# Optimization experiments

Measured on AMD Instinct MI355X. Metric: run time of the kernel, lower is better.

Reference implementation:

```python
import jax, jax.numpy as jnp
import numpy as np

B, K, G, C = 64, 4000, 200, 91
LAMBDA_BOX, LAMBDA_CLS, LAMBDA_OBJ = 5.0, 1.0, 1.0
EPS = 1e-9


def _make_boxes(key, lead_shape):
    k1, k2 = jax.random.split(key)
    tl = jax.random.uniform(k1, lead_shape + (2,)) * 0.7
    wh = jax.random.uniform(k2, lead_shape + (2,)) * 0.29 + 0.01
    return jnp.concatenate([tl, tl + wh], axis=-1)


def setup_inputs() -> dict:
    key = jax.random.key(0)
    ks = jax.random.split(key, 6)
    pred_boxes = _make_boxes(ks[0], (B, K))
    pred_obj_logits = jax.random.normal(ks[1], (B, K), dtype=jnp.float32)
    pred_cls_logits = jax.random.normal(ks[2], (B, K, C), dtype=jnp.float32)
    gt_boxes = _make_boxes(ks[3], (B, G))
    gt_labels = jax.random.randint(ks[4], (B, G), 0, C)
    n_gt = jax.random.randint(ks[5], (B,), 1, G + 1)
    gt_mask = jnp.arange(G)[None, :] < n_gt[:, None]
    return dict(pred_boxes=pred_boxes, pred_obj_logits=pred_obj_logits,
                pred_cls_logits=pred_cls_logits, gt_boxes=gt_boxes,
                gt_labels=gt_labels, gt_mask=gt_mask)


def _area(x):
    return jnp.clip(x[..., 2] - x[..., 0], 0.0) * jnp.clip(x[..., 3] - x[..., 1], 0.0)


def _pairwise_iou(a, b):
    # a: (K,4), b: (G,4) -> (K,G)
    tl = jnp.maximum(a[:, None, :2], b[None, :, :2])
    br = jnp.minimum(a[:, None, 2:], b[None, :, 2:])
    wh = jnp.clip(br - tl, 0.0)
    inter = wh[..., 0] * wh[..., 1]
    union = jnp.clip(_area(a)[:, None] + _area(b)[None, :] - inter, EPS)
    return inter / union


def _ciou_loss(pb, gb):
    # pb, gb: (M,4) matched pairs; elementwise CIoU loss = 1 - CIoU
    tl = jnp.maximum(pb[:, :2], gb[:, :2])
    br = jnp.minimum(pb[:, 2:], gb[:, 2:])
    wh = jnp.clip(br - tl, 0.0)
    inter = wh[:, 0] * wh[:, 1]
    iou = inter / jnp.clip(_area(pb) + _area(gb) - inter, EPS)
    px = (pb[:, 0] + pb[:, 2]) * 0.5
    py = (pb[:, 1] + pb[:, 3]) * 0.5
    tx = (gb[:, 0] + gb[:, 2]) * 0.5
    ty = (gb[:, 1] + gb[:, 3]) * 0.5
    rho2 = (px - tx) ** 2 + (py - ty) ** 2
    etl = jnp.minimum(pb[:, :2], gb[:, :2])
    ebr = jnp.maximum(pb[:, 2:], gb[:, 2:])
    c2 = jnp.clip((ebr[:, 0] - etl[:, 0]) ** 2 + (ebr[:, 1] - etl[:, 1]) ** 2, EPS)
    pw = jnp.clip(pb[:, 2] - pb[:, 0], EPS)
    ph = jnp.clip(pb[:, 3] - pb[:, 1], EPS)
    tw = jnp.clip(gb[:, 2] - gb[:, 0], EPS)
    th = jnp.clip(gb[:, 3] - gb[:, 1], EPS)
    v = (4.0 / jnp.pi ** 2) * (jnp.arctan(tw / th) - jnp.arctan(pw / ph)) ** 2
    alpha = jax.lax.stop_gradient(v / (1.0 - iou + v + EPS))  # torch.no_grad
    return 1.0 - (iou - rho2 / c2 - alpha * v)


def _greedy_match(iou0):
    # iou0: (K,G), invalid gt columns pre-masked to -1. Fixed min(K,G)-step
    # argmax-and-mask scan reproducing the torch greedy loop (break -> valid=False).
    Gd = iou0.shape[1]
    steps = min(iou0.shape[0], Gd)

    def step(m, _):
        flat = jnp.argmax(m)
        p = flat // Gd
        g = flat % Gd
        valid = m.reshape(-1)[flat] >= 0.0
        m2 = m.at[p, :].set(-1.0).at[:, g].set(-1.0)
        return jnp.where(valid, m2, m), (p, g, valid)

    _, (ps, gs, vs) = jax.lax.scan(step, iou0, None, length=steps)
    return ps, gs, vs


def _per_batch(pred_b, cls_b, gt_b, labels_b, mask_b):
    iou = jax.lax.stop_gradient(_pairwise_iou(pred_b, gt_b))  # matching is non-diff (.item() in torch)
    iou = jnp.where(mask_b[None, :], iou, -1.0)
    ps, gs, vs = _greedy_match(iou)
    vf = vs.astype(pred_b.dtype)
    n = jnp.sum(vf)
    denom = jnp.maximum(n, 1.0)
    pb = pred_b[ps]
    gb = gt_b[gs]
    lbox = jnp.sum(_ciou_loss(pb, gb) * vf) / denom
    logp = jax.nn.log_softmax(cls_b[ps], axis=-1)
    lce = -jnp.take_along_axis(logp, labels_b[gs][:, None], axis=1)[:, 0]
    lcls = jnp.sum(lce * vf) / denom
    obj_tgt = jnp.zeros((pred_b.shape[0],), pred_b.dtype).at[
        jnp.where(vs, ps, pred_b.shape[0])].set(1.0, mode='drop')
    return lbox, lcls, obj_tgt, n > 0.0


def reference(pred_boxes, pred_obj_logits, pred_cls_logits, gt_boxes, gt_labels, gt_mask):
    lbox_b, lcls_b, obj_tgt, has = jax.vmap(_per_batch)(
        pred_boxes, pred_cls_logits, gt_boxes, gt_labels, gt_mask)
    hf = has.astype(pred_boxes.dtype)
    nb = jnp.maximum(jnp.sum(hf), 1.0)
    loss_box = jnp.sum(lbox_b * hf) / nb
    loss_cls = jnp.sum(lcls_b * hf) / nb
    # BCEWithLogits(mean): softplus(x) - t*x
    loss_obj = jnp.mean(jax.nn.softplus(pred_obj_logits) - obj_tgt * pred_obj_logits)
    total = LAMBDA_BOX * loss_box + LAMBDA_CLS * loss_cls + LAMBDA_OBJ * loss_obj
    return total, loss_box, loss_cls, loss_obj
```

## Files before the change

kernel.cpp:

```cpp
#include <hip/hip_runtime.h>
#include <math.h>

#define B_ 64
#define K_ 4000
#define G_ 200
#define C_ 91
#define EPS_ 1e-9f
#define NW_ 16
#define DEPTH_ 32
typedef unsigned long long ull;

#define WS_FLAG 0
#define WS_PART 256
#define WS_TOP 65536

__device__ __forceinline__ float box_area(float4 a) {
#pragma clang fp contract(off)
  return fmaxf(a.z - a.x, 0.f) * fmaxf(a.w - a.y, 0.f);
}

__device__ __forceinline__ float iou_ab(float4 a, float aA, float4 b, float aB) {
#pragma clang fp contract(off)
  float tlx = fmaxf(a.x, b.x), tly = fmaxf(a.y, b.y);
  float brx = fminf(a.z, b.z), bry = fminf(a.w, b.w);
  float w = fmaxf(brx - tlx, 0.f), h = fmaxf(bry - tly, 0.f);
  float inter = w * h;
  float uni = fmaxf(aA + aB - inter, EPS_);
  return inter / uni;
}

__device__ __forceinline__ float ciou_loss(float4 p, float4 g) {
  float tlx = fmaxf(p.x, g.x), tly = fmaxf(p.y, g.y);
  float brx = fminf(p.z, g.z), bry = fminf(p.w, g.w);
  float w = fmaxf(brx - tlx, 0.f), h = fmaxf(bry - tly, 0.f);
  float inter = w * h;
  float areaP = fmaxf(p.z - p.x, 0.f) * fmaxf(p.w - p.y, 0.f);
  float areaG = fmaxf(g.z - g.x, 0.f) * fmaxf(g.w - g.y, 0.f);
  float iou = inter / fmaxf(areaP + areaG - inter, EPS_);
  float px = (p.x + p.z) * 0.5f, py = (p.y + p.w) * 0.5f;
  float tx = (g.x + g.z) * 0.5f, ty = (g.y + g.w) * 0.5f;
  float rho2 = (px - tx) * (px - tx) + (py - ty) * (py - ty);
  float ex = fmaxf(p.z, g.z) - fminf(p.x, g.x);
  float ey = fmaxf(p.w, g.w) - fminf(p.y, g.y);
  float c2 = fmaxf(ex * ex + ey * ey, EPS_);
  float pw = fmaxf(p.z - p.x, EPS_), ph = fmaxf(p.w - p.y, EPS_);
  float tw = fmaxf(g.z - g.x, EPS_), th = fmaxf(g.w - g.y, EPS_);
  float dat = atanf(tw / th) - atanf(pw / ph);
  float v = (4.0f / (float)(M_PI * M_PI)) * dat * dat;
  float alpha = v / ((1.f - iou) + v + EPS_);
  return 1.f - (iou - rho2 / c2 - alpha * v);
}

__global__ void kdetect(const unsigned char* m8, int* flag) {
  int b = threadIdx.x;
  int ok = 1;
  const unsigned char* r = m8 + b * G_;
  if (r[0] != 1) ok = 0;
  int seen0 = 0;
  for (int g = 0; g < G_; ++g) {
    unsigned char c = r[g];
    if (c > 1) { ok = 0; break; }
    if (c == 0) seen0 = 1;
    else if (seen0) { ok = 0; break; }
  }
  int all = __all(ok);
  if (b == 0) *flag = all ? 1 : 0;
}

__device__ __forceinline__ float block_sum(float v, float* s_red) {
  for (int off = 32; off > 0; off >>= 1) v += __shfl_xor(v, off);
  int lane = threadIdx.x & 63, wid = threadIdx.x >> 6;
  if (lane == 0) s_red[wid] = v;
  __syncthreads();
  float r = 0.f;
  if (wid == 0) {
    float t = (lane < NW_) ? s_red[lane] : 0.f;
    for (int off = 32; off > 0; off >>= 1) t += __shfl_xor(t, off);
    r = t;
  }
  __syncthreads();
  return r;
}

__device__ __forceinline__ void merge4_stage(ull& v0, ull& v1, ull& v2, ull& v3,
                                             int off) {
  ull w0 = __shfl_xor(v0, off), w1 = __shfl_xor(v1, off);
  ull w2 = __shfl_xor(v2, off), w3 = __shfl_xor(v3, off);
  ull t0 = v0 > w3 ? v0 : w3;
  ull t1 = v1 > w2 ? v1 : w2;
  ull t2 = v2 > w1 ? v2 : w1;
  ull t3 = v3 > w0 ? v3 : w0;
  ull x;
  if (t2 > t0) { x = t0; t0 = t2; t2 = x; }
  if (t3 > t1) { x = t1; t1 = t3; t3 = x; }
  if (t1 > t0) { x = t0; t0 = t1; t1 = x; }
  if (t3 > t2) { x = t2; t2 = t3; t3 = x; }
  v0 = t0; v1 = t1; v2 = t2; v3 = t3;
}

#define TOP4_INS(key, t0, t1, t2, t3)                   \
  if ((key) > t3) {                                     \
    t3 = (key);                                         \
    ull tmp_;                                           \
    if (t3 > t2) { tmp_ = t2; t2 = t3; t3 = tmp_; }     \
    if (t2 > t1) { tmp_ = t1; t1 = t2; t2 = tmp_; }     \
    if (t1 > t0) { tmp_ = t0; t0 = t1; t1 = tmp_; }     \
  }

__device__ __forceinline__ void rank_extract(ull t0, ull t1, ull t2, ull t3,
                                             ull* dst, int lane) {
  int r0 = 0, r1 = 0, r2 = 0, r3 = 0;
  for (int i = 0; i < 64; ++i) {
    ull o0 = __shfl(t0, i), o1 = __shfl(t1, i);
    ull o2 = __shfl(t2, i), o3 = __shfl(t3, i);
    r0 += (o0 > t0) + (o1 > t0) + (o2 > t0) + (o3 > t0);
    r1 += (o0 > t1) + (o1 > t1) + (o2 > t1) + (o3 > t1);
    r2 += (o0 > t2) + (o1 > t2) + (o2 > t2) + (o3 > t2);
    r3 += (o0 > t3) + (o1 > t3) + (o2 > t3) + (o3 > t3);
  }
  int cut = (t3 != 0ull) ? (r3 + 1) : 0x7FFFFFFF;
  int nc = (t0 != 0ull) + (t1 != 0ull) + (t2 != 0ull) + (t3 != 0ull);
  for (int off = 32; off > 0; off >>= 1) {
    int oc = __shfl_xor(cut, off);
    cut = (oc < cut) ? oc : cut;
    nc += __shfl_xor(nc, off);
  }
  const int Lf = (cut < DEPTH_) ? cut : DEPTH_;
  const int zstart = (Lf < nc) ? Lf : nc;
  if (t0 != 0ull && r0 < Lf) dst[r0] = t0;
  if (t1 != 0ull && r1 < Lf) dst[r1] = t1;
  if (t2 != 0ull && r2 < Lf) dst[r2] = t2;
  if (t3 != 0ull && r3 < Lf) dst[r3] = t3;
  for (int o = lane; o < DEPTH_; o += 64)
    if (o >= zstart) dst[o] = 0ull;
}

__global__ __launch_bounds__(1024) void kinit(const float* __restrict__ pred_boxes,
                                              const float* __restrict__ gt_boxes,
                                              const void* __restrict__ gt_mask,
                                              char* __restrict__ ws) {
  const int wv = blockIdx.x * 16 + (threadIdx.x >> 6);
  const int lane = threadIdx.x & 63;
  const int b = wv / 100, j = wv - 100 * b;
  const int c0 = 2 * j, c1 = 2 * j + 1;
  const int msk8 = *(const int*)(ws + WS_FLAG);
  const float4* p4 = (const float4*)pred_boxes + (size_t)b * K_;
  const float4* g4 = (const float4*)gt_boxes + (size_t)b * G_;

  int vA, vB;
  if (msk8) {
    vA = ((const unsigned char*)gt_mask)[(size_t)b * G_ + c0] != 0;
    vB = ((const unsigned char*)gt_mask)[(size_t)b * G_ + c1] != 0;
  } else {
    vA = ((const int*)gt_mask)[(size_t)b * G_ + c0] != 0;
    vB = ((const int*)gt_mask)[(size_t)b * G_ + c1] != 0;
  }
  if (!(vA | vB)) return;

  float4 gbA, gbB;
  float gAA = 0.f, gAB = 0.f;
  if (vA) { gbA = g4[c0]; gAA = box_area(gbA); }
  if (vB) { gbB = g4[c1]; gAB = box_area(gbB); }

  ull a0 = 0, a1 = 0, a2 = 0, a3 = 0;
  ull b0 = 0, b1 = 0, b2 = 0, b3 = 0;
#pragma unroll 4
  for (int k = lane; k < K_; k += 64) {
    float4 pb = p4[k];
    float ar = box_area(pb);
    if (vA) {
      float iou = iou_ab(pb, ar, gbA, gAA);
      ull e = ((ull)__float_as_uint(iou) << 12) | (ull)(4095 - k);
      TOP4_INS(e, a0, a1, a2, a3);
    }
    if (vB) {
      float iou = iou_ab(pb, ar, gbB, gAB);
      ull e = ((ull)__float_as_uint(iou) << 12) | (ull)(4095 - k);
      TOP4_INS(e, b0, b1, b2, b3);
    }
  }
  ull* wtop = (ull*)(ws + WS_TOP);
  if (vA) rank_extract(a0, a1, a2, a3, wtop + ((size_t)b * G_ + c0) * DEPTH_, lane);
  if (vB) rank_extract(b0, b1, b2, b3, wtop + ((size_t)b * G_ + c1) * DEPTH_, lane);
}

__global__ __launch_bounds__(1024) void kmerged(
    const float* __restrict__ pred_boxes, const float* __restrict__ obj_logits,
    const float* __restrict__ cls_logits, const float* __restrict__ gt_boxes,
    const int* __restrict__ gt_labels, const void* __restrict__ gt_mask,
    char* __restrict__ ws) {
  __shared__ float s_gx[G_], s_gy[G_], s_gz[G_], s_gw[G_], s_garea[G_];
  __shared__ unsigned char s_valid[G_];
  __shared__ unsigned char s_rowused[4096];
  __shared__ ull s_tlkey[G_][DEPTH_ + 1];
  __shared__ unsigned short s_tlrow[G_][DEPTH_ + 1];
  __shared__ int s_mp[G_];
  __shared__ unsigned short s_mg[G_];
  __shared__ int s_cnt;
  __shared__ float s_red[NW_];
  const int b = blockIdx.x;
  const int tid = threadIdx.x, lane = tid & 63, wid = tid >> 6;
  const int msk8 = *(const int*)(ws + WS_FLAG);
  const float4* p4 = (const float4*)pred_boxes + (size_t)b * K_;
  const float4* g4 = (const float4*)gt_boxes + (size_t)b * G_;
  const ull* wtop = (const ull*)(ws + WS_TOP);

  for (int g = tid; g < G_; g += 1024) {
    float4 gb = g4[g];
    s_gx[g] = gb.x; s_gy[g] = gb.y; s_gz[g] = gb.z; s_gw[g] = gb.w;
    s_garea[g] = box_area(gb);
    int v;
    if (msk8) v = ((const unsigned char*)gt_mask)[(size_t)b * G_ + g] != 0;
    else      v = ((const int*)gt_mask)[(size_t)b * G_ + g] != 0;
    s_valid[g] = (unsigned char)v;
  }
  for (int k = tid; k < 4096; k += 1024) s_rowused[k] = 0;
  __syncthreads();
  for (int i = tid; i < G_ * DEPTH_; i += 1024) {
    int col = i >> 5, o = i & 31;
    ull v = s_valid[col] ? wtop[(size_t)b * G_ * DEPTH_ + i] : 0ull;
    s_tlkey[col][o] = v;
    s_tlrow[col][o] = v ? (unsigned short)(4095 - (int)((v >> 12) & 0xFFF))
                        : (unsigned short)0xFFFF;
  }
  __syncthreads();

  if (wid == 0) {
    ull key0 = 0, key1 = 0, key2 = 0, key3 = 0;
    int ptr0 = DEPTH_, ptr1 = DEPTH_, ptr2 = DEPTH_, ptr3 = DEPTH_;
    int cloc = 0;
#define SLOTINIT(S)                                                        \
    { int col = S * 64 + lane;                                             \
      if (col < G_) {                                                      \
        ull h_ = s_tlkey[col][0];                                          \
        if (h_ != 0ull) {                                                  \
          key##S = (h_ << 8) | (ull)(255 - col); ptr##S = 1; ++cloc; } } }
    SLOTINIT(0) SLOTINIT(1) SLOTINIT(2) SLOTINIT(3)
#undef SLOTINIT
    for (int off = 32; off > 0; off >>= 1) cloc += __shfl_xor(cloc, off);
    const int cnt = cloc;
    if (lane == 0) s_cnt = cnt;

    for (int step = 0; step < cnt;) {
      ull v0 = key0, v1 = key1, v2 = key2, v3 = key3, x;
      if (v1 > v0) { x = v0; v0 = v1; v1 = x; }
      if (v3 > v2) { x = v2; v2 = v3; v3 = x; }
      if (v2 > v0) { x = v0; v0 = v2; v2 = x; }
      if (v3 > v1) { x = v1; v1 = v3; v3 = x; }
      if (v2 > v1) { x = v1; v1 = v2; v2 = x; }
      merge4_stage(v0, v1, v2, v3, 32);
      merge4_stage(v0, v1, v2, v3, 16);
      merge4_stage(v0, v1, v2, v3, 8);
      merge4_stage(v0, v1, v2, v3, 4);
      merge4_stage(v0, v1, v2, v3, 2);
      merge4_stage(v0, v1, v2, v3, 1);
      const int P0 = 4095 - (int)((v0 >> 8) & 0xFFF), G0 = 255 - (int)(v0 & 0xFF);
      const int P1 = 4095 - (int)((v1 >> 8) & 0xFFF), G1 = 255 - (int)(v1 & 0xFF);
      const int P2 = 4095 - (int)((v2 >> 8) & 0xFFF), G2 = 255 - (int)(v2 & 0xFF);
      const int P3 = 4095 - (int)((v3 >> 8) & 0xFFF), G3 = 255 - (int)(v3 & 0xFF);
      const int lim = cnt - step;
      const bool a2 = (v1 != 0ull) && (P1 != P0) && (lim > 1);
      const bool a3 = a2 && (v2 != 0ull) && (P2 != P0) && (P2 != P1) && (lim > 2);
      const bool a4 = a3 && (v3 != 0ull) && (P3 != P0) && (P3 != P1) && (P3 != P2) && (lim > 3);
      const int nacc = 1 + (int)a2 + (int)a3 + (int)a4;
      if (lane == 0) {
        s_mp[step] = P0; s_mg[step] = (unsigned short)G0; s_rowused[P0] = 1;
        if (a2) { s_mp[step + 1] = P1; s_mg[step + 1] = (unsigned short)G1; s_rowused[P1] = 1; }
        if (a3) { s_mp[step + 2] = P2; s_mg[step + 2] = (unsigned short)G2; s_rowused[P2] = 1; }
        if (a4) { s_mp[step + 3] = P3; s_mg[step + 3] = (unsigned short)G3; s_rowused[P3] = 1; }
      }
      __builtin_amdgcn_wave_barrier();
      const int gA = G0, gB = a2 ? G1 : -1, gC = a3 ? G2 : -1, gD = a4 ? G3 : -1;
      const int pA = P0, pB = a2 ? P1 : -1, pC = a3 ? P2 : -1, pD = a4 ? P3 : -1;
      int need = 0;
#define DEMOTE(S)                                                           \
      { int col = S * 64 + lane; ull kk = key##S;                           \
        if (kk != 0ull) {                                                   \
          if (col == gA || col == gB || col == gC || col == gD) {           \
            key##S = 0ull;                                                  \
          } else {                                                          \
            int krow = 4095 - (int)((kk >> 8) & 0xFFF);                     \
            if (krow == pA || krow == pB || krow == pC || krow == pD) {     \
              ull nk = 0ull; int np = ptr##S;                               \
              while (np < DEPTH_) {                                         \
                int r_ = s_tlrow[col][np];                                  \
                if (r_ == 0xFFFF) { np = DEPTH_; break; }                   \
                if (!s_rowused[r_]) {                                       \
                  nk = (s_tlkey[col][np] << 8) | (ull)(255 - col);          \
                  ++np; break;                                              \
                }                                                           \
                ++np;                                                       \
              }                                                             \
              ptr##S = np; key##S = nk;                                     \
              if (nk == 0ull) need |= (1 << S); } } } }
      DEMOTE(0) DEMOTE(1) DEMOTE(2) DEMOTE(3)
#undef DEMOTE
      while (__any(need)) {
        unsigned long long bal = __ballot(need != 0);
        int src = (int)__builtin_ctzll(bal);
        int myslot = need ? __builtin_ctz(need) : 0;
        int slot = __shfl(myslot, src);
        int col = slot * 64 + src;
        float4 gb = make_float4(s_gx[col], s_gy[col], s_gz[col], s_gw[col]);
        float gA2 = s_garea[col];
        ull t0 = 0, t1 = 0, t2 = 0, t3 = 0;
#pragma unroll 2
        for (int k = lane; k < K_; k += 64) {
          if (!s_rowused[k]) {
            float4 pb = p4[k];
            float iou = iou_ab(pb, box_area(pb), gb, gA2);
            ull e = ((ull)__float_as_uint(iou) << 12) | (ull)(4095 - k);
            TOP4_INS(e, t0, t1, t2, t3);
          }
        }
        int r0 = 0, r1 = 0, r2 = 0, r3 = 0;
        for (int i = 0; i < 64; ++i) {
          ull o0 = __shfl(t0, i), o1 = __shfl(t1, i);
          ull o2 = __shfl(t2, i), o3 = __shfl(t3, i);
          r0 += (o0 > t0) + (o1 > t0) + (o2 > t0) + (o3 > t0);
          r1 += (o0 > t1) + (o1 > t1) + (o2 > t1) + (o3 > t1);
          r2 += (o0 > t2) + (o1 > t2) + (o2 > t2) + (o3 > t2);
          r3 += (o0 > t3) + (o1 > t3) + (o2 > t3) + (o3 > t3);
        }
        int cut = (t3 != 0ull) ? (r3 + 1) : 0x7FFFFFFF;
        int nc = (t0 != 0ull) + (t1 != 0ull) + (t2 != 0ull) + (t3 != 0ull);
        for (int off = 32; off > 0; off >>= 1) {
          int oc = __shfl_xor(cut, off);
          cut = (oc < cut) ? oc : cut;
          nc += __shfl_xor(nc, off);
        }
        const int Lf = (cut < DEPTH_) ? cut : DEPTH_;
        const int zstart = (Lf < nc) ? Lf : nc;
        if (t0 != 0ull && r0 < Lf) {
          s_tlkey[col][r0] = t0;
          s_tlrow[col][r0] = (unsigned short)(4095 - (int)((t0 >> 12) & 0xFFF));
        }
        if (t1 != 0ull && r1 < Lf) {
          s_tlkey[col][r1] = t1;
          s_tlrow[col][r1] = (unsigned short)(4095 - (int)((t1 >> 12) & 0xFFF));
        }
        if (t2 != 0ull && r2 < Lf) {
          s_tlkey[col][r2] = t2;
          s_tlrow[col][r2] = (unsigned short)(4095 - (int)((t2 >> 12) & 0xFFF));
        }
        if (t3 != 0ull && r3 < Lf) {
          s_tlkey[col][r3] = t3;
          s_tlrow[col][r3] = (unsigned short)(4095 - (int)((t3 >> 12) & 0xFFF));
        }
        for (int o = lane; o < DEPTH_; o += 64)
          if (o >= zstart) { s_tlkey[col][o] = 0ull; s_tlrow[col][o] = 0xFFFF; }
        __builtin_amdgcn_wave_barrier();
        ull newhead = s_tlkey[col][0];
        if (lane == src) {
          ull nk = (newhead << 8) | (ull)(255 - col);
          if (slot == 0) { key0 = nk; ptr0 = 1; }
          else if (slot == 1) { key1 = nk; ptr1 = 1; }
          else if (slot == 2) { key2 = nk; ptr2 = 1; }
          else { key3 = nk; ptr3 = 1; }
          need &= ~(1 << slot);
        }
        __builtin_amdgcn_wave_barrier();
      }
      step += nacc;
    }
  }
  __syncthreads();

  const int cnt = s_cnt;
  float lbox = 0.f, lcls = 0.f;
  for (int i = tid; i < cnt; i += 1024) {
    int p = s_mp[i], g = s_mg[i];
    float4 pb = p4[p];
    float4 gb = make_float4(s_gx[g], s_gy[g], s_gz[g], s_gw[g]);
    lbox += ciou_loss(pb, gb);
    int label = gt_labels[(size_t)b * G_ + g];
    const float* lg = cls_logits + ((size_t)b * K_ + p) * C_;
    float m = -1e30f;
    for (int cc = 0; cc < C_; ++cc) m = fmaxf(m, lg[cc]);
    float s = 0.f;
    for (int cc = 0; cc < C_; ++cc) s += expf(lg[cc] - m);
    lcls += (m + logf(s)) - lg[label];
  }
  float obj = 0.f;
  const float* ol = obj_logits + (size_t)b * K_;
  for (int k = tid; k < K_; k += 1024) {
    float x = ol[k];
    float sp = fmaxf(x, 0.f) + log1pf(expf(-fabsf(x)));
    if (s_rowused[k]) sp -= x;
    obj += sp;
  }
  lbox = block_sum(lbox, s_red);
  lcls = block_sum(lcls, s_red);
  obj = block_sum(obj, s_red);
  if (tid == 0) {
    float* partials = (float*)(ws + WS_PART);
    float n = (float)cnt;
    float denom = fmaxf(n, 1.f);
    partials[b * 4 + 0] = lbox / denom;
    partials[b * 4 + 1] = lcls / denom;
    partials[b * 4 + 2] = obj;
    partials[b * 4 + 3] = (n > 0.f) ? 1.f : 0.f;
  }
}

__global__ void kfinal(const char* __restrict__ ws, float* __restrict__ out) {
  int b = threadIdx.x;
  const float* partials = (const float*)(ws + WS_PART);
  float lb = partials[b * 4 + 0], lc = partials[b * 4 + 1];
  float ob = partials[b * 4 + 2], hf = partials[b * 4 + 3];
  float sb = lb * hf, sc = lc * hf, sh = hf, so = ob;
  for (int off = 32; off > 0; off >>= 1) {
    sb += __shfl_xor(sb, off);
    sc += __shfl_xor(sc, off);
    sh += __shfl_xor(sh, off);
    so += __shfl_xor(so, off);
  }
  if (b == 0) {
    float nb = fmaxf(sh, 1.f);
    float box = sb / nb, cls = sc / nb;
    float obj = so / (float)(B_ * K_);
    out[0] = 5.f * box + cls + obj;
    out[1] = box;
    out[2] = cls;
    out[3] = obj;
  }
}

extern "C" void kernel_launch(void* const* d_in, const int* in_sizes, int n_in,
                              void* d_out, int out_size, void* d_ws, size_t ws_size,
                              hipStream_t stream) {
  const float* pred_boxes = (const float*)d_in[0];
  const float* obj_logits = (const float*)d_in[1];
  const float* cls_logits = (const float*)d_in[2];
  const float* gt_boxes = (const float*)d_in[3];
  const int* gt_labels = (const int*)d_in[4];
  const void* gt_mask = d_in[5];
  float* out = (float*)d_out;
  char* ws = (char*)d_ws;

  hipLaunchKernelGGL(kdetect, dim3(1), dim3(64), 0, stream,
                     (const unsigned char*)gt_mask, (int*)(ws + WS_FLAG));
  hipLaunchKernelGGL(kinit, dim3(400), dim3(1024), 0, stream,
                     pred_boxes, gt_boxes, gt_mask, ws);
  hipLaunchKernelGGL(kmerged, dim3(B_), dim3(1024), 0, stream,
                     pred_boxes, obj_logits, cls_logits, gt_boxes, gt_labels,
                     gt_mask, ws);
  hipLaunchKernelGGL(kfinal, dim3(1), dim3(64), 0, stream, ws, out);
}
```

Measured before the change: 293.2 us.

## Stage pred boxes in LDS for top-k init and widen greedy merge to eight

The init kernel now gives each block one batch and 25 GT columns, and stages that batch's 4000 pred boxes in shared memory so each wave reads them from LDS rather than global memory. Invalid columns now get their top-list explicitly zeroed. In the greedy matching loop, the wave-wide bitonic merge keeps the top 8 candidates instead of 4, so up to 8 non-conflicting matches can be accepted per iteration. This cuts the number of serial iterations in exchange for twice the shuffles and compares per iteration.

```diff
diff --git a/kernel.cpp b/kernel.cpp
--- a/kernel.cpp
+++ b/kernel.cpp
@@ -82,20 +82,34 @@
   return r;
 }
 
-__device__ __forceinline__ void merge4_stage(ull& v0, ull& v1, ull& v2, ull& v3,
-                                             int off) {
-  ull w0 = __shfl_xor(v0, off), w1 = __shfl_xor(v1, off);
-  ull w2 = __shfl_xor(v2, off), w3 = __shfl_xor(v3, off);
-  ull t0 = v0 > w3 ? v0 : w3;
-  ull t1 = v1 > w2 ? v1 : w2;
-  ull t2 = v2 > w1 ? v2 : w1;
-  ull t3 = v3 > w0 ? v3 : w0;
+__device__ __forceinline__ void merge8_stage(ull* v, int off) {
+  ull w0 = __shfl_xor(v[0], off), w1 = __shfl_xor(v[1], off);
+  ull w2 = __shfl_xor(v[2], off), w3 = __shfl_xor(v[3], off);
+  ull w4 = __shfl_xor(v[4], off), w5 = __shfl_xor(v[5], off);
+  ull w6 = __shfl_xor(v[6], off), w7 = __shfl_xor(v[7], off);
+  ull t0 = v[0] > w7 ? v[0] : w7;
+  ull t1 = v[1] > w6 ? v[1] : w6;
+  ull t2 = v[2] > w5 ? v[2] : w5;
+  ull t3 = v[3] > w4 ? v[3] : w4;
+  ull t4 = v[4] > w3 ? v[4] : w3;
+  ull t5 = v[5] > w2 ? v[5] : w2;
+  ull t6 = v[6] > w1 ? v[6] : w1;
+  ull t7 = v[7] > w0 ? v[7] : w0;
   ull x;
+  if (t4 > t0) { x = t0; t0 = t4; t4 = x; }
+  if (t5 > t1) { x = t1; t1 = t5; t5 = x; }
+  if (t6 > t2) { x = t2; t2 = t6; t6 = x; }
+  if (t7 > t3) { x = t3; t3 = t7; t7 = x; }
   if (t2 > t0) { x = t0; t0 = t2; t2 = x; }
   if (t3 > t1) { x = t1; t1 = t3; t3 = x; }
+  if (t6 > t4) { x = t4; t4 = t6; t6 = x; }
+  if (t7 > t5) { x = t5; t5 = t7; t7 = x; }
   if (t1 > t0) { x = t0; t0 = t1; t1 = x; }
   if (t3 > t2) { x = t2; t2 = t3; t3 = x; }
-  v0 = t0; v1 = t1; v2 = t2; v3 = t3;
+  if (t5 > t4) { x = t4; t4 = t5; t5 = x; }
+  if (t7 > t6) { x = t6; t6 = t7; t7 = x; }
+  v[0] = t0; v[1] = t1; v[2] = t2; v[3] = t3;
+  v[4] = t4; v[5] = t5; v[6] = t6; v[7] = t7;
 }
 
 #define TOP4_INS(key, t0, t1, t2, t3)                   \
@@ -139,49 +153,65 @@
                                               const float* __restrict__ gt_boxes,
                                               const void* __restrict__ gt_mask,
                                               char* __restrict__ ws) {
-  const int wv = blockIdx.x * 16 + (threadIdx.x >> 6);
-  const int lane = threadIdx.x & 63;
-  const int b = wv / 100, j = wv - 100 * b;
-  const int c0 = 2 * j, c1 = 2 * j + 1;
+  __shared__ float4 s_p[K_];
+  const int blk = blockIdx.x;
+  const int b = blk >> 3, oct = blk & 7;
+  const int tid = threadIdx.x, lane = tid & 63, wid = tid >> 6;
   const int msk8 = *(const int*)(ws + WS_FLAG);
   const float4* p4 = (const float4*)pred_boxes + (size_t)b * K_;
   const float4* g4 = (const float4*)gt_boxes + (size_t)b * G_;
 
-  int vA, vB;
-  if (msk8) {
-    vA = ((const unsigned char*)gt_mask)[(size_t)b * G_ + c0] != 0;
-    vB = ((const unsigned char*)gt_mask)[(size_t)b * G_ + c1] != 0;
-  } else {
-    vA = ((const int*)gt_mask)[(size_t)b * G_ + c0] != 0;
-    vB = ((const int*)gt_mask)[(size_t)b * G_ + c1] != 0;
-  }
-  if (!(vA | vB)) return;
+  for (int i = tid; i < K_; i += 1024) s_p[i] = p4[i];
+  __syncthreads();
+
+  const int base = oct * 25;
+  const int colA = base + wid;
+  const int colB = base + 16 + wid;
+  const bool hasB = (wid < 9);
+  ull* wtop = (ull*)(ws + WS_TOP);
+
+  int vA, vB = 0;
+  if (msk8) vA = ((const unsigned char*)gt_mask)[(size_t)b * G_ + colA] != 0;
+  else      vA = ((const int*)gt_mask)[(size_t)b * G_ + colA] != 0;
+  if (hasB) {
+    if (msk8) vB = ((const unsigned char*)gt_mask)[(size_t)b * G_ + colB] != 0;
+    else      vB = ((const int*)gt_mask)[(size_t)b * G_ + colB] != 0;
+  }
 
   float4 gbA, gbB;
   float gAA = 0.f, gAB = 0.f;
-  if (vA) { gbA = g4[c0]; gAA = box_area(gbA); }
-  if (vB) { gbB = g4[c1]; gAB = box_area(gbB); }
+  if (vA) { gbA = g4[colA]; gAA = box_area(gbA); }
+  if (vB) { gbB = g4[colB]; gAB = box_area(gbB); }
 
   ull a0 = 0, a1 = 0, a2 = 0, a3 = 0;
   ull b0 = 0, b1 = 0, b2 = 0, b3 = 0;
-#pragma unroll 4
-  for (int k = lane; k < K_; k += 64) {
-    float4 pb = p4[k];
-    float ar = box_area(pb);
-    if (vA) {
-      float iou = iou_ab(pb, ar, gbA, gAA);
-      ull e = ((ull)__float_as_uint(iou) << 12) | (ull)(4095 - k);
-      TOP4_INS(e, a0, a1, a2, a3);
+  if (vA | vB) {
+#pragma unroll 2
+    for (int k = lane; k < K_; k += 64) {
+      float4 pb = s_p[k];
+      float ar = box_area(pb);
+      if (vA) {
+        float iou = iou_ab(pb, ar, gbA, gAA);
+        ull e = ((ull)__float_as_uint(iou) << 12) | (ull)(4095 - k);
+        TOP4_INS(e, a0, a1, a2, a3);
+      }
+      if (vB) {
+        float iou = iou_ab(pb, ar, gbB, gAB);
+        ull e = ((ull)__float_as_uint(iou) << 12) | (ull)(4095 - k);
+        TOP4_INS(e, b0, b1, b2, b3);
+      }
     }
-    if (vB) {
-      float iou = iou_ab(pb, ar, gbB, gAB);
-      ull e = ((ull)__float_as_uint(iou) << 12) | (ull)(4095 - k);
-      TOP4_INS(e, b0, b1, b2, b3);
-    }
-  }
-  ull* wtop = (ull*)(ws + WS_TOP);
-  if (vA) rank_extract(a0, a1, a2, a3, wtop + ((size_t)b * G_ + c0) * DEPTH_, lane);
-  if (vB) rank_extract(b0, b1, b2, b3, wtop + ((size_t)b * G_ + c1) * DEPTH_, lane);
+  }
+  {
+    ull* dstA = wtop + ((size_t)b * G_ + colA) * DEPTH_;
+    if (vA) rank_extract(a0, a1, a2, a3, dstA, lane);
+    else    for (int o = lane; o < DEPTH_; o += 64) dstA[o] = 0ull;
+  }
+  if (hasB) {
+    ull* dstB = wtop + ((size_t)b * G_ + colB) * DEPTH_;
+    if (vB) rank_extract(b0, b1, b2, b3, dstB, lane);
+    else    for (int o = lane; o < DEPTH_; o += 64) dstB[o] = 0ull;
+  }
 }
 
 __global__ __launch_bounds__(1024) void kmerged(
@@ -242,45 +272,68 @@
     if (lane == 0) s_cnt = cnt;
 
     for (int step = 0; step < cnt;) {
-      ull v0 = key0, v1 = key1, v2 = key2, v3 = key3, x;
-      if (v1 > v0) { x = v0; v0 = v1; v1 = x; }
-      if (v3 > v2) { x = v2; v2 = v3; v3 = x; }
-      if (v2 > v0) { x = v0; v0 = v2; v2 = x; }
-      if (v3 > v1) { x = v1; v1 = v3; v3 = x; }
-      if (v2 > v1) { x = v1; v1 = v2; v2 = x; }
-      merge4_stage(v0, v1, v2, v3, 32);
-      merge4_stage(v0, v1, v2, v3, 16);
-      merge4_stage(v0, v1, v2, v3, 8);
-      merge4_stage(v0, v1, v2, v3, 4);
-      merge4_stage(v0, v1, v2, v3, 2);
-      merge4_stage(v0, v1, v2, v3, 1);
-      const int P0 = 4095 - (int)((v0 >> 8) & 0xFFF), G0 = 255 - (int)(v0 & 0xFF);
-      const int P1 = 4095 - (int)((v1 >> 8) & 0xFFF), G1 = 255 - (int)(v1 & 0xFF);
-      const int P2 = 4095 - (int)((v2 >> 8) & 0xFFF), G2 = 255 - (int)(v2 & 0xFF);
-      const int P3 = 4095 - (int)((v3 >> 8) & 0xFFF), G3 = 255 - (int)(v3 & 0xFF);
+      ull v[8];
+      {
+        ull q0 = key0, q1 = key1, q2 = key2, q3 = key3, x;
+        if (q1 > q0) { x = q0; q0 = q1; q1 = x; }
+        if (q3 > q2) { x = q2; q2 = q3; q3 = x; }
+        if (q2 > q0) { x = q0; q0 = q2; q2 = x; }
+        if (q3 > q1) { x = q1; q1 = q3; q3 = x; }
+        if (q2 > q1) { x = q1; q1 = q2; q2 = x; }
+        v[0] = q0; v[1] = q1; v[2] = q2; v[3] = q3;
+        v[4] = 0; v[5] = 0; v[6] = 0; v[7] = 0;
+      }
+      merge8_stage(v, 32);
+      merge8_stage(v, 16);
+      merge8_stage(v, 8);
+      merge8_stage(v, 4);
+      merge8_stage(v, 2);
+      merge8_stage(v, 1);
+      int P[8], Gc[8];
+#pragma unroll
+      for (int i = 0; i < 8; ++i) {
+        P[i] = 4095 - (int)((v[i] >> 8) & 0xFFF);
+        Gc[i] = 255 - (int)(v[i] & 0xFF);
+      }
       const int lim = cnt - step;
-      const bool a2 = (v1 != 0ull) && (P1 != P0) && (lim > 1);
-      const bool a3 = a2 && (v2 != 0ull) && (P2 != P0) && (P2 != P1) && (lim > 2);
-      const bool a4 = a3 && (v3 != 0ull) && (P3 != P0) && (P3 != P1) && (P3 != P2) && (lim > 3);
-      const int nacc = 1 + (int)a2 + (int)a3 + (int)a4;
+      bool okp = true;
+      int nacc = 0;
+      int gacc[8], pacc[8];
+#pragma unroll
+      for (int i = 0; i < 8; ++i) {
+        bool d = (v[i] != 0ull) && (lim > i);
+#pragma unroll
+        for (int j = 0; j < 8; ++j)
+          if (j < i) d = d && (P[i] != P[j]);
+        okp = okp && d;
+        gacc[i] = okp ? Gc[i] : -1;
+        pacc[i] = okp ? P[i] : -1;
+        if (okp) ++nacc;
+      }
       if (lane == 0) {
-        s_mp[step] = P0; s_mg[step] = (unsigned short)G0; s_rowused[P0] = 1;
-        if (a2) { s_mp[step + 1] = P1; s_mg[step + 1] = (unsigned short)G1; s_rowused[P1] = 1; }
-        if (a3) { s_mp[step + 2] = P2; s_mg[step + 2] = (unsigned short)G2; s_rowused[P2] = 1; }
-        if (a4) { s_mp[step + 3] = P3; s_mg[step + 3] = (unsigned short)G3; s_rowused[P3] = 1; }
+#pragma unroll
+        for (int i = 0; i < 8; ++i)
+          if (i < nacc) {
+            s_mp[step + i] = P[i];
+            s_mg[step + i] = (unsigned short)Gc[i];
+            s_rowused[P[i]] = 1;
+          }
       }
       __builtin_amdgcn_wave_barrier();
-      const int gA = G0, gB = a2 ? G1 : -1, gC = a3 ? G2 : -1, gD = a4 ? G3 : -1;
-      const int pA = P0, pB = a2 ? P1 : -1, pC = a3 ? P2 : -1, pD = a4 ? P3 : -1;
       int need = 0;
 #define DEMOTE(S)                                                           \
       { int col = S * 64 + lane; ull kk = key##S;                           \
         if (kk != 0ull) {                                                   \
-          if (col == gA || col == gB || col == gC || col == gD) {           \
-            key##S = 0ull;                                                  \
-          } else {                                                          \
+          bool kill = false;                                                \
+          _Pragma("unroll") for (int i = 0; i < 8; ++i)                     \
+            kill |= (col == gacc[i]);                                       \
+          if (kill) { key##S = 0ull; }                                      \
+          else {                                                            \
             int krow = 4095 - (int)((kk >> 8) & 0xFFF);                     \
-            if (krow == pA || krow == pB || krow == pC || krow == pD) {     \
+            bool stale = false;                                             \
+            _Pragma("unroll") for (int i = 0; i < 8; ++i)                   \
+              stale |= (krow == pacc[i]);                                   \
+            if (stale) {                                                    \
               ull nk = 0ull; int np = ptr##S;                               \
               while (np < DEPTH_) {                                         \
                 int r_ = s_tlrow[col][np];                                  \
@@ -440,7 +493,7 @@
 
   hipLaunchKernelGGL(kdetect, dim3(1), dim3(64), 0, stream,
                      (const unsigned char*)gt_mask, (int*)(ws + WS_FLAG));
-  hipLaunchKernelGGL(kinit, dim3(400), dim3(1024), 0, stream,
+  hipLaunchKernelGGL(kinit, dim3(B_ * 8), dim3(1024), 0, stream,
                      pred_boxes, gt_boxes, gt_mask, ws);
   hipLaunchKernelGGL(kmerged, dim3(B_), dim3(1024), 0, stream,
                      pred_boxes, obj_logits, cls_logits, gt_boxes, gt_labels,
```

Measured after the change: 273.3 us. 1.07x faster.
